# Kernel tuning notes

Hardware: AMD Instinct MI355X
Metric: run time of the kernel (lower is better)

## Reference

```python
import jax, jax.numpy as jnp
import numpy as np

N = 4096
INPUT_DIM = 256
HIDDEN = 64
HEADS = 8
NEG_SLOPE = 0.2
MASK_FILL = -10000.0


def setup_inputs() -> dict:
    key = jax.random.key(0)
    k_x, k_adj, k_w, k_as, k_ad = jax.random.split(key, 5)
    x = jax.random.normal(k_x, (N, INPUT_DIM), dtype=jnp.float32)
    adjacency = jax.random.bernoulli(k_adj, 0.05, (N, N)) | jnp.eye(N, dtype=bool)
    # linear weight, torch convention: [out_features, in_features]
    W = jax.random.normal(k_w, (HEADS * HIDDEN, INPUT_DIM), dtype=jnp.float32) * 0.05
    attn_src = jax.random.normal(k_as, (HEADS, HIDDEN), dtype=jnp.float32) * 0.1
    attn_dst = jax.random.normal(k_ad, (HEADS, HIDDEN), dtype=jnp.float32) * 0.1
    return {"x": x, "adjacency": adjacency, "W": W, "attn_src": attn_src, "attn_dst": attn_dst}


def reference(x, adjacency, W, attn_src, attn_dst):
    # h: [N, heads, hidden]
    h = (x @ W.T).reshape(N, HEADS, HIDDEN)
    src_scores = jnp.einsum('nhd,hd->nh', h, attn_src)  # [N, heads]
    dst_scores = jnp.einsum('nhd,hd->nh', h, attn_dst)  # [N, heads]
    # logits[i, j, h] = src[i, h] + dst[j, h]  (matches torch permute(2,0,1) layout math)
    logits = src_scores[:, None, :] + dst_scores[None, :, :]  # [N, N, heads]
    logits = jax.nn.leaky_relu(logits, negative_slope=NEG_SLOPE)
    logits = jnp.where(adjacency[:, :, None], logits, MASK_FILL)
    alpha = jax.nn.softmax(logits, axis=1)  # softmax over source nodes j
    out = jnp.einsum('ijh,jhf->ihf', alpha, h)  # [N, heads, hidden]
    return out.mean(axis=1)  # [N, hidden]
```

## Files before the change

### kernel.cpp

```cpp
#include <hip/hip_runtime.h>

#define NN 4096
#define IN_DIM 256
#define HID 64
#define HEADS 8

typedef __attribute__((ext_vector_type(4))) float f32x4;
typedef __attribute__((ext_vector_type(8))) short s16x8;
typedef unsigned short u16;
typedef unsigned long long u64;

__device__ inline u16 f2bf(float f) {
  union { float f; unsigned u; } v; v.f = f;
  unsigned r = (v.u + 0x7FFFu + ((v.u >> 16) & 1u)) >> 16;
  return (u16)r;
}
__device__ inline float bf2f(u16 b) {
  union { unsigned u; float f; } v; v.u = ((unsigned)b) << 16;
  return v.f;
}
__device__ __forceinline__ unsigned cvt_pk_bf16(float a, float b) {
  unsigned r;
  asm("v_cvt_pk_bf16_f32 %0, %1, %2" : "=v"(r) : "v"(a), "v"(b));
  return r;
}

__global__ void gat_detect(const void* __restrict__ adj, int* __restrict__ flag)
{
  const int lane = threadIdx.x;
  const unsigned char* a8 = (const unsigned char*)adj;
  const int* a32 = (const int*)adj;

  size_t i8 = (size_t)(4 * lane + 1) * 4097;
  int p8 = a8[i8] != 0;

  size_t k = (size_t)(2 * lane + 1);
  int p32 = a32[k * 4097] != 0;
  int p64 = a32[2 * k * 4097] != 0;

  int ok8 = __all(p8), ok32 = __all(p32), ok64 = __all(p64);
  if (lane == 0) *flag = ok8 ? 0 : (ok32 ? 1 : (ok64 ? 2 : 1));
}

__global__ __launch_bounds__(256) void gat_pack(
    const void* __restrict__ adj, const int* __restrict__ flag,
    u64* __restrict__ bits)
{
  const int mode = *flag;
  const int lane = threadIdx.x & 63;
  const int wave = (blockIdx.x * blockDim.x + threadIdx.x) >> 6;
  const int nwaves = (gridDim.x * blockDim.x) >> 6;
  const size_t nwords = (size_t)NN * NN / 64;

  for (size_t w = wave; w < nwords; w += nwaves) {
    size_t e = w * 64 + lane;
    int on;
    if (mode == 1)      on = ((const int*)adj)[e] != 0;
    else if (mode == 0) on = ((const unsigned char*)adj)[e] != 0;
    else                on = ((const long long*)adj)[e] != 0;
    u64 b = __ballot(on);
    if (lane == 0) bits[w] = b;
  }
}

__global__ __launch_bounds__(256) void gat_gemm1(
    const float* __restrict__ x, const float* __restrict__ W,
    const float* __restrict__ a_src, const float* __restrict__ a_dst,
    u16* __restrict__ Hbt, float* __restrict__ s_srcT,
    float* __restrict__ s_dstT)
{
  __shared__ u16 xhi[64 * 72], xlo[64 * 72], whi[64 * 72], wlo[64 * 72];
  const int nb = blockIdx.x;
  const int ob = blockIdx.y;
  const int t = threadIdx.x;
  const int lane = t & 63, wid = t >> 6;
  const int wr = wid >> 1, wc = wid & 1;
  const int g = lane >> 4;

  f32x4 acc[2][2] = {};

  const int sn = t >> 2;
  const int skc = (t & 3) * 16;

  for (int kb = 0; kb < 4; ++kb) {
    const float* xr = x + (size_t)(nb * 64 + sn) * IN_DIM + kb * 64 + skc;
    const float* wr_p = W + (size_t)(ob * 64 + sn) * IN_DIM + kb * 64 + skc;
#pragma unroll
    for (int c = 0; c < 4; ++c) {
      float4 xv = ((const float4*)xr)[c];
      float4 wv = ((const float4*)wr_p)[c];
      float xf[4] = {xv.x, xv.y, xv.z, xv.w};
      float wf[4] = {wv.x, wv.y, wv.z, wv.w};
      u16 xh[4], xl[4], wh[4], wl[4];
#pragma unroll
      for (int e = 0; e < 4; ++e) {
        xh[e] = f2bf(xf[e]); xl[e] = f2bf(xf[e] - bf2f(xh[e]));
        wh[e] = f2bf(wf[e]); wl[e] = f2bf(wf[e] - bf2f(wh[e]));
      }
      int base = sn * 72 + skc + c * 4;
      *(ushort4*)(xhi + base) = make_ushort4(xh[0], xh[1], xh[2], xh[3]);
      *(ushort4*)(xlo + base) = make_ushort4(xl[0], xl[1], xl[2], xl[3]);
      *(ushort4*)(whi + base) = make_ushort4(wh[0], wh[1], wh[2], wh[3]);
      *(ushort4*)(wlo + base) = make_ushort4(wl[0], wl[1], wl[2], wl[3]);
    }
    __syncthreads();
#pragma unroll
    for (int ks = 0; ks < 2; ++ks) {
      const int k0 = ks * 32 + g * 8;
      s16x8 ah[2], al[2], bh[2], bl[2];
#pragma unroll
      for (int nf = 0; nf < 2; ++nf) {
        int row = wr * 32 + nf * 16 + (lane & 15);
        ah[nf] = *(const s16x8*)(xhi + row * 72 + k0);
        al[nf] = *(const s16x8*)(xlo + row * 72 + k0);
      }
#pragma unroll
      for (int of = 0; of < 2; ++of) {
        int row = wc * 32 + of * 16 + (lane & 15);
        bh[of] = *(const s16x8*)(whi + row * 72 + k0);
        bl[of] = *(const s16x8*)(wlo + row * 72 + k0);
      }
#pragma unroll
      for (int nf = 0; nf < 2; ++nf)
#pragma unroll
        for (int of = 0; of < 2; ++of) {
          acc[nf][of] = __builtin_amdgcn_mfma_f32_16x16x32_bf16(ah[nf], bh[of], acc[nf][of], 0, 0, 0);
          acc[nf][of] = __builtin_amdgcn_mfma_f32_16x16x32_bf16(ah[nf], bl[of], acc[nf][of], 0, 0, 0);
          acc[nf][of] = __builtin_amdgcn_mfma_f32_16x16x32_bf16(al[nf], bh[of], acc[nf][of], 0, 0, 0);
        }
    }
    __syncthreads();
  }

  u16* Ct = xhi;
#pragma unroll
  for (int nf = 0; nf < 2; ++nf)
#pragma unroll
    for (int of = 0; of < 2; ++of)
#pragma unroll
      for (int r = 0; r < 4; ++r) {
        int nloc = wr * 32 + nf * 16 + g * 4 + r;
        int oloc = wc * 32 + of * 16 + (lane & 15);
        Ct[oloc * 72 + nloc] = f2bf(acc[nf][of][r]);
      }

  {
    const float* asp = a_src + ob * 64;
    const float* adp = a_dst + ob * 64;
    float as0 = asp[wc * 32 + (lane & 15)], as1 = asp[wc * 32 + 16 + (lane & 15)];
    float ad0 = adp[wc * 32 + (lane & 15)], ad1 = adp[wc * 32 + 16 + (lane & 15)];
    float* sred = (float*)wlo;
#pragma unroll
    for (int nf = 0; nf < 2; ++nf)
#pragma unroll
      for (int r = 0; r < 4; ++r) {
        float vs = acc[nf][0][r] * as0 + acc[nf][1][r] * as1;
        float vd = acc[nf][0][r] * ad0 + acc[nf][1][r] * ad1;
#pragma unroll
        for (int m = 1; m < 16; m <<= 1) { vs += __shfl_xor(vs, m); vd += __shfl_xor(vd, m); }
        if ((lane & 15) == 0) {
          int node = wr * 32 + nf * 16 + g * 4 + r;
          sred[wc * 64 + node] = vs;
          sred[128 + wc * 64 + node] = vd;
        }
      }
  }
  __syncthreads();
  {
    int o = t >> 2, nc = (t & 3) * 16;
    u16* dst = Hbt + ((size_t)(ob * 64 + nb) * 64 + o) * 64 + nc;
#pragma unroll
    for (int c = 0; c < 2; ++c) {
      s16x8 v = *(const s16x8*)(Ct + o * 72 + nc + c * 8);
      *(s16x8*)(dst + c * 8) = v;
    }
  }
  if (t < 64) {
    const float* sred = (const float*)wlo;
    s_srcT[(size_t)ob * NN + nb * 64 + t] = sred[t] + sred[64 + t];
    s_dstT[(size_t)ob * NN + nb * 64 + t] = sred[128 + t] + sred[192 + t];
  }
}

__global__ __launch_bounds__(512) void gat_dmax(
    const float* __restrict__ s_dstT, float* __restrict__ Mh)
{
  const int w = threadIdx.x >> 6, lane = threadIdx.x & 63;
  const float* p = s_dstT + (size_t)w * NN;
  float m = -INFINITY;
#pragma unroll
  for (int it = 0; it < 16; ++it) {
    f32x4 v = *(const f32x4*)(p + (it * 64 + lane) * 4);
    m = fmaxf(fmaxf(fmaxf(m, v[0]), v[1]), fmaxf(v[2], v[3]));
  }
#pragma unroll
  for (int s = 1; s < 64; s <<= 1) m = fmaxf(m, __shfl_xor(m, s));
  if (lane == 0) Mh[w] = m;
}

__global__ __launch_bounds__(512, 4) void gat_flash(
    const u64* __restrict__ bits, const u16* __restrict__ Hbt,
    const float* __restrict__ s_srcT, const float* __restrict__ s_dstT,
    const float* __restrict__ Mh, float* __restrict__ pout)
{
  __shared__ char shmem[17408];
  __shared__ float Lbuf[8][16];
  u16* Ast = (u16*)shmem;
  float (*Mbuf)[16][66] = (float(*)[16][66])shmem;

  const int t = threadIdx.x, lane = t & 63, wid = t >> 6;
  const int ws4 = wid & 3, jh = wid >> 2;
  const int bid = blockIdx.x;
  const int h = bid & 7, iblk = bid >> 3;
  const int i_loc = lane & 15, g = lane >> 4, j0 = g * 8;
  const int irow = iblk * 64 + ws4 * 16 + i_loc;

  const float s_i = s_srcT[(size_t)h * NN + irow];
  float m_i = s_i + Mh[h];
  m_i = fmaxf(m_i, 0.2f * m_i);
  const float L2E = 1.44269504f;
  const float mL = m_i * L2E;

  const u16* tile0 = Hbt + (size_t)h * 64 * 4096;
  const float* dT = s_dstT + (size_t)h * NN;
  const u64* brow = bits + (size_t)irow * 64;

  const int lt = t & 255;
  const int r0 = lt >> 3, colE = (lt & 7) * 8;
  const u16* gsrc0 = tile0 + r0 * 64 + (colE ^ ((r0 & 7) << 3));
  const int r1 = 32 + r0;
  const u16* gsrc1 = tile0 + r1 * 64 + (colE ^ ((r1 & 7) << 3));
  u16* sdst = Ast + jh * 4096;
  const char* lbase = (const char*)(Ast + jh * 4096);
  const int swz = (i_loc & 7) << 4;

  f32x4 acc[4] = {};
  f32x4 lacc = {0.f, 0.f, 0.f, 0.f};

#define QUAD(DV, MBITS, SH, PW0, PW1, LI) do {                        \
    float z0 = s_i + DV[0], z1 = s_i + DV[1];                         \
    float z2 = s_i + DV[2], z3 = s_i + DV[3];                         \
    z0 = fmaxf(z0, 0.2f * z0); z1 = fmaxf(z1, 0.2f * z1);             \
    z2 = fmaxf(z2, 0.2f * z2); z3 = fmaxf(z3, 0.2f * z3);             \
    float e0 = __builtin_amdgcn_exp2f(__builtin_fmaf(z0, L2E, -mL));  \
    float e1 = __builtin_amdgcn_exp2f(__builtin_fmaf(z1, L2E, -mL));  \
    float e2 = __builtin_amdgcn_exp2f(__builtin_fmaf(z2, L2E, -mL));  \
    float e3 = __builtin_amdgcn_exp2f(__builtin_fmaf(z3, L2E, -mL));  \
    e0 = ((MBITS >> (SH + 0)) & 1u) ? e0 : 0.f;                       \
    e1 = ((MBITS >> (SH + 1)) & 1u) ? e1 : 0.f;                       \
    e2 = ((MBITS >> (SH + 2)) & 1u) ? e2 : 0.f;                       \
    e3 = ((MBITS >> (SH + 3)) & 1u) ? e3 : 0.f;                       \
    lacc[LI] += (e0 + e1) + (e2 + e3);                                \
    PW0 = cvt_pk_bf16(e0, e1); PW1 = cvt_pk_bf16(e2, e3);             \
  } while (0)

  const int jt0 = jh * 32;
  u64 am_n = brow[jt0];
  f32x4 d_n0 = *(const f32x4*)(dT + jt0 * 64 + j0);
  f32x4 d_n1 = *(const f32x4*)(dT + jt0 * 64 + j0 + 4);
  f32x4 d_n2 = *(const f32x4*)(dT + jt0 * 64 + 32 + j0);
  f32x4 d_n3 = *(const f32x4*)(dT + jt0 * 64 + 36 + j0);

  for (int it = 0; it < 32; ++it) {
    const int jt = jt0 + it;
    s16x8 sv0 = *(const s16x8*)(gsrc0 + jt * 4096);
    s16x8 sv1 = *(const s16x8*)(gsrc1 + jt * 4096);

    const u64 am_ = am_n;
    f32x4 d0 = d_n0, d1 = d_n1, d2 = d_n2, d3 = d_n3;
    const int jn = jt0 + ((it + 1 < 32) ? it + 1 : 31);
    am_n = brow[jn];
    d_n0 = *(const f32x4*)(dT + jn * 64 + j0);
    d_n1 = *(const f32x4*)(dT + jn * 64 + j0 + 4);
    d_n2 = *(const f32x4*)(dT + jn * 64 + 32 + j0);
    d_n3 = *(const f32x4*)(dT + jn * 64 + 36 + j0);

    const unsigned amlo = (unsigned)(am_ >> j0);
    const unsigned amhi = (unsigned)(am_ >> (32 + j0));
    union { unsigned w_[4]; s16x8 v_; } P0, P1;
    QUAD(d0, amlo, 0, P0.w_[0], P0.w_[1], 0);
    QUAD(d1, amlo, 4, P0.w_[2], P0.w_[3], 1);
    QUAD(d2, amhi, 0, P1.w_[0], P1.w_[1], 2);
    QUAD(d3, amhi, 4, P1.w_[2], P1.w_[3], 3);

    __syncthreads();
    *(s16x8*)(sdst + lt * 8) = sv0;
    *(s16x8*)(sdst + 2048 + lt * 8) = sv1;
    __syncthreads();

#pragma unroll
    for (int fb = 0; fb < 4; ++fb) {
      const int rowb = (fb * 16 + i_loc) * 128;
      s16x8 A0 = *(const s16x8*)(lbase + rowb + ((g * 16) ^ swz));
      s16x8 A1 = *(const s16x8*)(lbase + rowb + (((g * 16) + 64) ^ swz));
      acc[fb] = __builtin_amdgcn_mfma_f32_16x16x32_bf16(A0, P0.v_, acc[fb], 0, 0, 0);
      acc[fb] = __builtin_amdgcn_mfma_f32_16x16x32_bf16(A1, P1.v_, acc[fb], 0, 0, 0);
    }
  }
#undef QUAD

  float l_run = (lacc[0] + lacc[1]) + (lacc[2] + lacc[3]);
  l_run += __shfl_xor(l_run, 16);
  l_run += __shfl_xor(l_run, 32);
  if (lane < 16) Lbuf[wid][i_loc] = l_run;

  __syncthreads();
  if (jh == 1) {
#pragma unroll
    for (int fb = 0; fb < 4; ++fb)
      *(f32x4*)&Mbuf[ws4][i_loc][fb * 16 + g * 4] = acc[fb];
  }
  __syncthreads();
  if (jh == 0) {
    const float invL = 1.f / (l_run + Lbuf[wid + 4][i_loc]);
    float* ob = pout + ((size_t)h * NN + irow) * 64;
#pragma unroll
    for (int fb = 0; fb < 4; ++fb) {
      f32x4 v = (acc[fb] + *(const f32x4*)&Mbuf[ws4][i_loc][fb * 16 + g * 4]) * invL;
      *(f32x4*)(ob + fb * 16 + g * 4) = v;
    }
  }
}

__global__ __launch_bounds__(256) void gat_combine(
    const float* __restrict__ pout, float* __restrict__ out)
{
  size_t e = (size_t)blockIdx.x * 256 + threadIdx.x;
  f32x4 s = {0.f, 0.f, 0.f, 0.f};
#pragma unroll
  for (int h = 0; h < 8; ++h)
    s += ((const f32x4*)pout)[(size_t)h * (NN * 16) + e];
  ((f32x4*)out)[e] = s * 0.125f;
}

extern "C" void kernel_launch(void* const* d_in, const int* in_sizes, int n_in,
                              void* d_out, int out_size, void* d_ws, size_t ws_size,
                              hipStream_t stream)
{
  const float* x = (const float*)d_in[0];
  const void* adj = d_in[1];
  const float* W = (const float*)d_in[2];
  const float* a_src = (const float*)d_in[3];
  const float* a_dst = (const float*)d_in[4];
  float* out = (float*)d_out;

  char* ws = (char*)d_ws;
  float* pout = (float*)ws;
  u16* Hbt = (u16*)(ws + 8 * 1024 * 1024);
  float* s_srcT = (float*)(ws + 12 * 1024 * 1024);
  float* s_dstT = (float*)(ws + 12 * 1024 * 1024 + 128 * 1024);
  int* flag = (int*)(ws + 12 * 1024 * 1024 + 256 * 1024);
  float* Mh = (float*)(ws + 12 * 1024 * 1024 + 384 * 1024);
  u64* bits = (u64*)(ws + 12 * 1024 * 1024 + 512 * 1024);

  gat_detect<<<1, 64, 0, stream>>>(adj, flag);
  gat_pack<<<2048, 256, 0, stream>>>(adj, flag, bits);
  gat_gemm1<<<dim3(64, 8), 256, 0, stream>>>(x, W, a_src, a_dst, Hbt, s_srcT, s_dstT);
  gat_dmax<<<1, 512, 0, stream>>>(s_dstT, Mh);
  gat_flash<<<512, 512, 0, stream>>>(bits, Hbt, s_srcT, s_dstT, Mh, pout);
  gat_combine<<<256, 256, 0, stream>>>(pout, out);
}
```

Before: 100.3 us.

## Split the attention j-range across four wave groups with double-buffered LDS tiles

The flash kernel now launches 1024 threads per block, and the source dimension is split into four quarters instead of two. Each wave group double-buffers its H tile in LDS and prefetches the next tile into registers, which leaves one barrier per iteration instead of two. Partial accumulators and row sums from the three extra groups are reduced through shared memory at the end. This adds latency hiding and parallelism, but it raises LDS use to about 64KB per block and tightens the register budget through the new launch bounds, so register spills are possible.

```diff
diff --git a/kernel.cpp b/kernel.cpp
--- a/kernel.cpp
+++ b/kernel.cpp
@@ -198,18 +198,17 @@
   if (lane == 0) Mh[w] = m;
 }
 
-__global__ __launch_bounds__(512, 4) void gat_flash(
+__global__ __launch_bounds__(1024, 8) void gat_flash(
     const u64* __restrict__ bits, const u16* __restrict__ Hbt,
     const float* __restrict__ s_srcT, const float* __restrict__ s_dstT,
     const float* __restrict__ Mh, float* __restrict__ pout)
 {
-  __shared__ char shmem[17408];
-  __shared__ float Lbuf[8][16];
+  __shared__ char shmem[65536];
+  __shared__ float Lbuf[16][16];
   u16* Ast = (u16*)shmem;
-  float (*Mbuf)[16][66] = (float(*)[16][66])shmem;
 
   const int t = threadIdx.x, lane = t & 63, wid = t >> 6;
-  const int ws4 = wid & 3, jh = wid >> 2;
+  const int ws4 = wid & 3, jq = wid >> 2;
   const int bid = blockIdx.x;
   const int h = bid & 7, iblk = bid >> 3;
   const int i_loc = lane & 15, g = lane >> 4, j0 = g * 8;
@@ -230,8 +229,6 @@
   const u16* gsrc0 = tile0 + r0 * 64 + (colE ^ ((r0 & 7) << 3));
   const int r1 = 32 + r0;
   const u16* gsrc1 = tile0 + r1 * 64 + (colE ^ ((r1 & 7) << 3));
-  u16* sdst = Ast + jh * 4096;
-  const char* lbase = (const char*)(Ast + jh * 4096);
   const int swz = (i_loc & 7) << 4;
 
   f32x4 acc[4] = {};
@@ -254,27 +251,28 @@
     PW0 = cvt_pk_bf16(e0, e1); PW1 = cvt_pk_bf16(e2, e3);             \
   } while (0)
 
-  const int jt0 = jh * 32;
-  u64 am_n = brow[jt0];
-  f32x4 d_n0 = *(const f32x4*)(dT + jt0 * 64 + j0);
-  f32x4 d_n1 = *(const f32x4*)(dT + jt0 * 64 + j0 + 4);
-  f32x4 d_n2 = *(const f32x4*)(dT + jt0 * 64 + 32 + j0);
-  f32x4 d_n3 = *(const f32x4*)(dT + jt0 * 64 + 36 + j0);
-
-  for (int it = 0; it < 32; ++it) {
-    const int jt = jt0 + it;
-    s16x8 sv0 = *(const s16x8*)(gsrc0 + jt * 4096);
-    s16x8 sv1 = *(const s16x8*)(gsrc1 + jt * 4096);
-
-    const u64 am_ = am_n;
-    f32x4 d0 = d_n0, d1 = d_n1, d2 = d_n2, d3 = d_n3;
-    const int jn = jt0 + ((it + 1 < 32) ? it + 1 : 31);
-    am_n = brow[jn];
-    d_n0 = *(const f32x4*)(dT + jn * 64 + j0);
-    d_n1 = *(const f32x4*)(dT + jn * 64 + j0 + 4);
-    d_n2 = *(const f32x4*)(dT + jn * 64 + 32 + j0);
-    d_n3 = *(const f32x4*)(dT + jn * 64 + 36 + j0);
-
+  const int jtb = jq * 16;
+  s16x8 sv0 = *(const s16x8*)(gsrc0 + jtb * 4096);
+  s16x8 sv1 = *(const s16x8*)(gsrc1 + jtb * 4096);
+
+#pragma unroll 2
+  for (int it = 0; it < 16; ++it) {
+    const int jt = jtb + it;
+    u16* sdst = Ast + jq * 8192 + (it & 1) * 4096;
+
+    *(s16x8*)(sdst + lt * 8) = sv0;
+    *(s16x8*)(sdst + 2048 + lt * 8) = sv1;
+    if (it < 15) {
+      sv0 = *(const s16x8*)(gsrc0 + (jt + 1) * 4096);
+      sv1 = *(const s16x8*)(gsrc1 + (jt + 1) * 4096);
+    }
+
+    const u64 am_ = brow[jt];
+    const float* dp = dT + jt * 64 + j0;
+    f32x4 d0 = *(const f32x4*)(dp);
+    f32x4 d1 = *(const f32x4*)(dp + 4);
+    f32x4 d2 = *(const f32x4*)(dp + 32);
+    f32x4 d3 = *(const f32x4*)(dp + 36);
     const unsigned amlo = (unsigned)(am_ >> j0);
     const unsigned amhi = (unsigned)(am_ >> (32 + j0));
     union { unsigned w_[4]; s16x8 v_; } P0, P1;
@@ -284,10 +282,8 @@
     QUAD(d3, amhi, 4, P1.w_[2], P1.w_[3], 3);
 
     __syncthreads();
-    *(s16x8*)(sdst + lt * 8) = sv0;
-    *(s16x8*)(sdst + 2048 + lt * 8) = sv1;
-    __syncthreads();
-
+
+    const char* lbase = (const char*)sdst;
 #pragma unroll
     for (int fb = 0; fb < 4; ++fb) {
       const int rowb = (fb * 16 + i_loc) * 128;
@@ -305,19 +301,25 @@
   if (lane < 16) Lbuf[wid][i_loc] = l_run;
 
   __syncthreads();
-  if (jh == 1) {
+  float* accst = (float*)shmem;
+  if (jq != 0) {
+    float* ab = accst + (((jq - 1) * 4 + ws4) * 16 + i_loc) * 66;
 #pragma unroll
     for (int fb = 0; fb < 4; ++fb)
-      *(f32x4*)&Mbuf[ws4][i_loc][fb * 16 + g * 4] = acc[fb];
+      *(f32x4*)(ab + fb * 16 + g * 4) = acc[fb];
   }
   __syncthreads();
-  if (jh == 0) {
-    const float invL = 1.f / (l_run + Lbuf[wid + 4][i_loc]);
+  if (jq == 0) {
+    const float invL = 1.f / (l_run + Lbuf[ws4 + 4][i_loc] +
+                              Lbuf[ws4 + 8][i_loc] + Lbuf[ws4 + 12][i_loc]);
     float* ob = pout + ((size_t)h * NN + irow) * 64;
 #pragma unroll
     for (int fb = 0; fb < 4; ++fb) {
-      f32x4 v = (acc[fb] + *(const f32x4*)&Mbuf[ws4][i_loc][fb * 16 + g * 4]) * invL;
-      *(f32x4*)(ob + fb * 16 + g * 4) = v;
+      f32x4 v = acc[fb];
+#pragma unroll
+      for (int q = 0; q < 3; ++q)
+        v += *(const f32x4*)(accst + ((q * 4 + ws4) * 16 + i_loc) * 66 + fb * 16 + g * 4);
+      *(f32x4*)(ob + fb * 16 + g * 4) = v * invL;
     }
   }
 }
@@ -357,6 +359,6 @@
   gat_pack<<<2048, 256, 0, stream>>>(adj, flag, bits);
   gat_gemm1<<<dim3(64, 8), 256, 0, stream>>>(x, W, a_src, a_dst, Hbt, s_srcT, s_dstT);
   gat_dmax<<<1, 512, 0, stream>>>(s_dstT, Mh);
-  gat_flash<<<512, 512, 0, stream>>>(bits, Hbt, s_srcT, s_dstT, Mh, pout);
+  gat_flash<<<512, 1024, 0, stream>>>(bits, Hbt, s_srcT, s_dstT, Mh, pout);
   gat_combine<<<256, 256, 0, stream>>>(pout, out);
 }
```

Result: slower. 171.6 us (+71.2%).
